# Kernel optimization log

Hardware: AMD Instinct MI355X
Metric: run time of the kernel (lower is better)

## Reference

```python
import jax, jax.numpy as jnp
import numpy as np

M, N, P, T = 8000, 63, 64, 5


def setup_inputs() -> dict:
    key = jax.random.key(0)
    ks = jax.random.split(key, 19)
    sn = (1.0 / N) ** 0.5
    sp = (1.0 / P) ** 0.5
    f32 = jnp.float32
    return {
        "A": jax.random.normal(ks[0], (1, M, N), f32),
        "b": jax.random.normal(ks[1], (1, M), f32),
        "c": jax.random.normal(ks[2], (1, N), f32),
        "theta1r": sn * jax.random.normal(ks[3], (P, N + 1), f32),
        "theta1c": sn * jax.random.normal(ks[4], (P, N + 1), f32),
        "theta2rr": sp * jax.random.normal(ks[5], (P, P), f32),
        "theta2rc": sp * jax.random.normal(ks[6], (P, P), f32),
        "theta2cr": sp * jax.random.normal(ks[7], (P, P), f32),
        "theta3rr": sp * jax.random.normal(ks[8], (P, P), f32),
        "theta3rc": sp * jax.random.normal(ks[9], (P, P), f32),
        "theta3cr": sp * jax.random.normal(ks[10], (P, P), f32),
        "theta4rr": sp * jax.random.normal(ks[11], (P,), f32),
        "theta4rc": sp * jax.random.normal(ks[12], (P,), f32),
        "theta4cr": sp * jax.random.normal(ks[13], (P,), f32),
        "theta6r": sp * jax.random.normal(ks[14], (P, P), f32),
        "theta6c": sp * jax.random.normal(ks[15], (P, P), f32),
        "theta7": sp * jax.random.normal(ks[16], (P, P), f32),
        "W8": 0.05 * jax.random.normal(ks[17], (2, 2 * P), f32),
        "b8": 0.05 * jax.random.normal(ks[18], (2,), f32),
        "z": 7,
    }


def reference(A, b, c, theta1r, theta1c, theta2rr, theta2rc, theta2cr,
              theta3rr, theta3rc, theta3cr, theta4rr, theta4rc, theta4cr,
              theta6r, theta6c, theta7, W8, b8, z):
    relu = jax.nn.relu
    m, n = A.shape[1], A.shape[2]
    p = theta1r.shape[0]
    # raw node features: row node v -> [A[v,:], b[v]]; column node m -> [c, 0]
    Fr_raw = jnp.concatenate([A[0], b[0][:, None]], axis=1)        # (m, n+1)
    fc_raw = jnp.concatenate([c[0], jnp.zeros((1,), A.dtype)])     # (n+1,)
    Fr = Fr_raw / jnp.linalg.norm(Fr_raw, axis=1, keepdims=True)   # f(v), v < m
    fc = fc_raw / jnp.linalg.norm(fc_raw)                          # f(m)
    # edge weights w(v,u) = f(v).f(u) are detached in the original (float(...data))
    Frd = jax.lax.stop_gradient(Fr)
    fcd = jax.lax.stop_gradient(fc)
    Wrr = Frd @ Frd.T                                              # (m, m)
    dg = jnp.diagonal(Wrr)
    srr_pos = relu(Wrr).sum(axis=1) - relu(dg)                     # sum over u != v
    srr_neg = relu(-Wrr).sum(axis=1) - relu(-dg)
    wrc = Frd @ fcd                                                # (m,) = w(v, m)
    # identity: sum_u relu(t4 * w_u) = relu(t4) * sum_u relu(w_u) + relu(-t4) * sum_u relu(-w_u)
    Srr = relu(theta4rr)[:, None] * srr_pos[None, :] + relu(-theta4rr)[:, None] * srr_neg[None, :]
    Src = relu(theta4rc)[:, None] * relu(wrc)[None, :] + relu(-theta4rc)[:, None] * relu(-wrc)[None, :]
    scr = relu(theta4cr) * relu(wrc).sum() + relu(-theta4cr) * relu(-wrc).sum()
    edge_r = theta3rr @ Srr + theta3rc @ Src                       # (p, m), constant over t
    edge_c = theta3cr @ scr                                        # (p,)
    fz = Fr[z]                                                     # z < m: row node feature
    t1r = theta1r @ fz                                             # (p,)
    t1c = theta1c @ fz
    # mu init (p, m+1) = [[Ab^T, c0^T]; 0]; split into row columns / column node
    mu_r0 = jnp.zeros((p, m), A.dtype).at[: n + 1].set(Fr_raw.T)
    mu_c0 = jnp.zeros((p,), A.dtype).at[: n + 1].set(fc_raw)

    def step(carry, _):
        mu_r, mu_c = carry
        # row nodes: term2rr uses old mu[:, v]; term2rc uses old mu[:, m]
        new_r = relu(t1r[:, None] + theta2rr @ mu_r + (theta2rc @ mu_c)[:, None] + edge_r)
        # column node updated last within a sweep -> sees updated row embeddings
        new_c = relu(t1c + theta2cr @ new_r.sum(axis=1) + edge_c)
        return (new_r, new_c), None

    (mu_r, mu_c), _ = jax.lax.scan(step, (mu_r0, mu_c0), None, length=T)
    term6 = theta6r @ mu_r.sum(axis=1) + theta6c @ mu_c            # (p,)
    term7 = theta7 @ mu_r[:, z]                                    # (p,)
    feat = jax.nn.sigmoid(jnp.concatenate([term6, term7]))         # (2p,)
    return (feat @ W8.T + b8)[None, :]                             # (1, 2)
```

## Files before the change

kernel.cpp:

```cpp
#include <hip/hip_runtime.h>
#include <math.h>

typedef __attribute__((ext_vector_type(8))) short short8;
typedef __attribute__((ext_vector_type(4))) float f32x4;

#define WS_SPART 0
#define WS_GPART 262144
#define WS_WPART 294912
#define WS_CPART 295936
#define WS_T1R   335936
#define WS_T1C   336000
#define WS_AL    336064
#define WS_BE    336128
#define WS_GA    336192
#define WS_DE    336256
#define WS_ECP   336320
#define WS_ECN   336384
#define WS_W     336448
#define WS_MUZ   336512
#define WS_WSUM  336576
#define WS_RNORM 336640
#define WS_R2H   344832
#define WS_R2L   346880
#define WS_E4    348928
#define WS_FH    380928
#define WS_FL    643072

__device__ __forceinline__ float waveReduceSum(float v) {
#pragma unroll
    for (int m = 32; m >= 1; m >>= 1) v += __shfl_xor(v, m, 64);
    return v;
}
__device__ __forceinline__ unsigned short f2bf(float f) {
    unsigned int u = __float_as_uint(f);
    unsigned int r = (u + 0x7fffu + ((u >> 16) & 1u)) >> 16;
    return (unsigned short)r;
}
__device__ __forceinline__ float bf2f(unsigned short h) {
    return __uint_as_float(((unsigned int)h) << 16);
}

__global__ __launch_bounds__(256) void k_fr(
    const float* __restrict__ A, const float* __restrict__ b, const float* __restrict__ c,
    const float* __restrict__ th1r, const float* __restrict__ th1c,
    const float* __restrict__ th2rr, const float* __restrict__ th2rc,
    const float* __restrict__ th3rr, const float* __restrict__ th3rc, const float* __restrict__ th3cr,
    const float* __restrict__ th4rr, const float* __restrict__ th4rc, const float* __restrict__ th4cr,
    const int* __restrict__ zp,
    unsigned short* __restrict__ Fh, unsigned short* __restrict__ Fl,
    unsigned short* __restrict__ R2H, unsigned short* __restrict__ R2L,
    float* __restrict__ ws)
{
    int tid = threadIdx.x, lane = tid & 63, wid = tid >> 6;

    if (blockIdx.x == 512) {
        __shared__ float fcraw[64], fz[64], sh4a[64], sh4b[64];
        int p = lane;
        int z = zp[0];
        float cv = (p < 63) ? c[p] : 0.f;
        fcraw[p] = cv;
        float av = (p < 63) ? A[z * 63 + p] : b[z];
        float s2 = waveReduceSum(av * av);
        fz[p] = av * rsqrtf(s2);
        __syncthreads();

        float t1 = 0.f, t2 = 0.f, w0 = 0.f;
#pragma unroll 8
        for (int k = 0; k < 64; k++) {
            t1 += th1r[p * 64 + k] * fz[k];
            t2 += th1c[p * 64 + k] * fz[k];
            w0 += th2rc[p * 64 + k] * fcraw[k];
        }
        ws[WS_T1R + p] = t1;
        ws[WS_T1C + p] = t2;
        ws[WS_W + p] = t1 + w0;

        sh4a[p] = th4rr[p];
        sh4b[p] = th4rc[p];
        __syncthreads();
        float a = 0.f, bb = 0.f, g = 0.f, d = 0.f;
#pragma unroll 8
        for (int k = 0; k < 64; k++) {
            float t4 = sh4a[k];
            a  += th3rr[p * 64 + k] * fmaxf(t4, 0.f);
            bb += th3rr[p * 64 + k] * fmaxf(-t4, 0.f);
            float t5 = sh4b[k];
            g  += th3rc[p * 64 + k] * fmaxf(t5, 0.f);
            d  += th3rc[p * 64 + k] * fmaxf(-t5, 0.f);
        }
        ws[WS_AL + p] = a; ws[WS_BE + p] = bb;
        ws[WS_GA + p] = g; ws[WS_DE + p] = d;
        __syncthreads();
        sh4a[p] = th4cr[p];
        __syncthreads();
        float e1 = 0.f, e2 = 0.f;
#pragma unroll 8
        for (int k = 0; k < 64; k++) {
            float t6 = sh4a[k];
            e1 += th3cr[p * 64 + k] * fmaxf(t6, 0.f);
            e2 += th3cr[p * 64 + k] * fmaxf(-t6, 0.f);
        }
        ws[WS_ECP + p] = e1; ws[WS_ECN + p] = e2;

#pragma unroll
        for (int i = 0; i < 16; i++) {
            int idx = tid * 16 + i;
            float f = th2rr[idx];
            unsigned short h = f2bf(f);
            R2H[idx] = h;
            R2L[idx] = f2bf(f - bf2f(h));
        }
        return;
    }

    __shared__ float gsh[64];
    __shared__ float wsh2[2];
    if (tid < 64) gsh[tid] = 0.f;
    if (tid < 2) wsh2[tid] = 0.f;
    __syncthreads();

    float cv = (lane < 63) ? c[lane] : 0.f;
    float cn2 = waveReduceSum(cv * cv);
    float fcnl = cv * rsqrtf(cn2);

    int r0 = blockIdx.x * 16 + wid * 4;
    float gl = 0.f, lp = 0.f, ln = 0.f;
#pragma unroll
    for (int i = 0; i < 4; i++) {
        int r = r0 + i;
        if (r < 8000) {
            float val = (lane < 63) ? A[r * 63 + lane] : b[r];
            float s2 = waveReduceSum(val * val);
            float f = val * rsqrtf(s2);
            unsigned short h = f2bf(f);
            Fh[r * 64 + lane] = h;
            Fl[r * 64 + lane] = f2bf(f - bf2f(h));
            gl += f;
            float w = waveReduceSum(f * fcnl);
            if (lane == 0) {
                ws[WS_RNORM + r] = sqrtf(s2);
                lp += fmaxf(w, 0.f); ln += fmaxf(-w, 0.f);
            }
        } else {
            Fh[r * 64 + lane] = 0;
            Fl[r * 64 + lane] = 0;
        }
    }
    atomicAdd(&gsh[lane], gl);
    if (lane == 0) { atomicAdd(&wsh2[0], lp); atomicAdd(&wsh2[1], ln); }
    __syncthreads();
    if (tid < 64) ws[WS_GPART + blockIdx.x * 64 + tid] = gsh[tid];
    if (tid == 64) ws[WS_WPART + blockIdx.x * 2 + 0] = wsh2[0];
    if (tid == 65) ws[WS_WPART + blockIdx.x * 2 + 1] = wsh2[1];
}

__global__ __launch_bounds__(256) void k_gram(
    const unsigned short* __restrict__ Fh, float* __restrict__ ws)
{
    int tid = threadIdx.x, lane = tid & 63, wid = tid >> 6;
    int m = lane & 15, quad = lane >> 4;
    int vbase = blockIdx.x * 256 + wid * 64;

    short8 AH[8];
#pragma unroll
    for (int pt = 0; pt < 4; pt++)
#pragma unroll
        for (int q = 0; q < 2; q++)
            AH[pt * 2 + q] = *(const short8*)(Fh + (vbase + pt * 16 + m) * 64 + q * 32 + quad * 8);

    float srr[16];
#pragma unroll
    for (int i = 0; i < 16; i++) srr[i] = 0.f;

    const int y = blockIdx.y;
    const int boff = m * 64 + quad * 8;
    short8 B0[2], B1[2];
#pragma unroll
    for (int q = 0; q < 2; q++)
        B0[q] = *(const short8*)(Fh + y * 16 * 64 + boff + q * 32);

#pragma unroll 1
    for (int k2 = 0; k2 < 8; k2++) {
        int jB1 = y + 32 * (2 * k2 + 1);
#pragma unroll
        for (int q = 0; q < 2; q++)
            B1[q] = *(const short8*)(Fh + jB1 * 16 * 64 + boff + q * 32);
#pragma unroll
        for (int pt = 0; pt < 4; pt++) {
            f32x4 a = {0.f, 0.f, 0.f, 0.f};
            a = __builtin_amdgcn_mfma_f32_16x16x32_bf16(AH[pt * 2 + 0], B0[0], a, 0, 0, 0);
            a = __builtin_amdgcn_mfma_f32_16x16x32_bf16(AH[pt * 2 + 1], B0[1], a, 0, 0, 0);
#pragma unroll
            for (int r = 0; r < 4; r++) srr[pt * 4 + r] += fmaxf(a[r], 0.f);
        }
        if (k2 < 7) {
            int jB0 = y + 32 * (2 * k2 + 2);
#pragma unroll
            for (int q = 0; q < 2; q++)
                B0[q] = *(const short8*)(Fh + jB0 * 16 * 64 + boff + q * 32);
        }
#pragma unroll
        for (int pt = 0; pt < 4; pt++) {
            f32x4 a = {0.f, 0.f, 0.f, 0.f};
            a = __builtin_amdgcn_mfma_f32_16x16x32_bf16(AH[pt * 2 + 0], B1[0], a, 0, 0, 0);
            a = __builtin_amdgcn_mfma_f32_16x16x32_bf16(AH[pt * 2 + 1], B1[1], a, 0, 0, 0);
#pragma unroll
            for (int r = 0; r < 4; r++) srr[pt * 4 + r] += fmaxf(a[r], 0.f);
        }
    }
#pragma unroll
    for (int pt = 0; pt < 4; pt++)
#pragma unroll
        for (int r = 0; r < 4; r++) {
            float s = srr[pt * 4 + r];
            s += __shfl_xor(s, 1, 64); s += __shfl_xor(s, 2, 64);
            s += __shfl_xor(s, 4, 64); s += __shfl_xor(s, 8, 64);
            if (m == 0)
                ws[WS_SPART + y * 8192 + vbase + pt * 16 + quad * 4 + r] = s;
        }
}

__global__ __launch_bounds__(256) void k_mu0(
    const float* __restrict__ c, float* __restrict__ ws,
    unsigned short* __restrict__ MH, unsigned short* __restrict__ ML,
    const unsigned short* __restrict__ R2H, const unsigned short* __restrict__ R2L)
{
    __shared__ float XF[64][68];
    __shared__ float red[256], colp[256];
    __shared__ __align__(16) float wS[64], alS[64], beS[64], gaS[64], deS[64];
    __shared__ float fcnS[64], gS[64], sprow[64];
    __shared__ __align__(16) float e4sh[256];
    int tid = threadIdx.x, lane = tid & 63, wid = tid >> 6;
    int m = lane & 15, quad = lane >> 4;
    int v0 = blockIdx.x * 64;
    int cw = wid * 16 + m;
    int v = v0 + cw;

    if (wid == 0) {
        float cv = (lane < 63) ? c[lane] : 0.f;
        float cn2 = waveReduceSum(cv * cv);
        fcnS[lane] = cv * rsqrtf(cn2);
        wS[lane] = ws[WS_W + lane];
    } else if (wid == 1) {
        alS[lane] = ws[WS_AL + lane]; beS[lane] = ws[WS_BE + lane];
        float wp = 0.f;
#pragma unroll
        for (int k = 0; k < 8; k++) wp += ws[WS_WPART + (lane + 64 * k) * 2];
        wp = waveReduceSum(wp);
        if (lane == 0) ws[WS_WSUM] = wp;
    } else if (wid == 2) {
        gaS[lane] = ws[WS_GA + lane]; deS[lane] = ws[WS_DE + lane];
        float wn = 0.f;
#pragma unroll
        for (int k = 0; k < 8; k++) wn += ws[WS_WPART + (lane + 64 * k) * 2 + 1];
        wn = waveReduceSum(wn);
        if (lane == 0) ws[WS_WSUM + 1] = wn;
    }
    float gv = 0.f;
#pragma unroll 8
    for (int bb = 0; bb < 128; bb++) gv += ws[WS_GPART + (wid * 128 + bb) * 64 + lane];
    red[tid] = gv;
    __syncthreads();
    if (tid < 64) gS[tid] = red[tid] + red[64 + tid] + red[128 + tid] + red[192 + tid];
    __syncthreads();
    float sv = 0.f;
#pragma unroll
    for (int y = wid * 8; y < wid * 8 + 8; y++) sv += ws[WS_SPART + y * 8192 + v0 + lane];
    red[tid] = sv;
    __syncthreads();
    if (tid < 64) sprow[tid] = red[tid] + red[64 + tid] + red[128 + tid] + red[192 + tid];
    __syncthreads();

    for (int i2 = 0; i2 < 16; i2++) {
        int i = wid * 16 + i2;
        int vr = v0 + i;
        float fr = bf2f(MH[vr * 64 + lane]) + bf2f(ML[vr * 64 + lane]);
        float dw = waveReduceSum(fr * fcnS[lane]);
        float dg = waveReduceSum(fr * gS[lane]);
        if (lane == 0) {
            float spv = sprow[i];
            float4 e;
            e.x = spv - 1.0f;
            e.y = spv - dg;
            e.z = fmaxf(dw, 0.f);
            e.w = fmaxf(-dw, 0.f);
            *(float4*)(&e4sh[i * 4]) = e;
            *(float4*)(ws + WS_E4 + vr * 4) = e;
        }
        XF[i][lane] = fr * ws[WS_RNORM + vr];
    }

    short8 RH[8], RL[8];
#pragma unroll
    for (int pt = 0; pt < 4; pt++)
#pragma unroll
        for (int q = 0; q < 2; q++) {
            int off = (pt * 16 + m) * 64 + q * 32 + quad * 8;
            RH[pt * 2 + q] = *(const short8*)(R2H + off);
            RL[pt * 2 + q] = *(const short8*)(R2L + off);
        }
    __syncthreads();

    short8 BH[2], BL[2];
#pragma unroll
    for (int q = 0; q < 2; q++) {
        float4 f0 = *(const float4*)(&XF[cw][q * 32 + quad * 8]);
        float4 f1 = *(const float4*)(&XF[cw][q * 32 + quad * 8 + 4]);
        float xv[8] = {f0.x, f0.y, f0.z, f0.w, f1.x, f1.y, f1.z, f1.w};
        short8 H, L;
#pragma unroll
        for (int j = 0; j < 8; j++) {
            unsigned short h = f2bf(xv[j]);
            H[j] = (short)h;
            L[j] = (short)f2bf(xv[j] - bf2f(h));
        }
        BH[q] = H; BL[q] = L;
    }
    float4 e = *(const float4*)(&e4sh[cw * 4]);

#pragma unroll
    for (int pt = 0; pt < 4; pt++) {
        f32x4 a = {0.f, 0.f, 0.f, 0.f};
#pragma unroll
        for (int q = 0; q < 2; q++) {
            a = __builtin_amdgcn_mfma_f32_16x16x32_bf16(RH[pt*2+q], BH[q], a, 0, 0, 0);
            a = __builtin_amdgcn_mfma_f32_16x16x32_bf16(RH[pt*2+q], BL[q], a, 0, 0, 0);
            a = __builtin_amdgcn_mfma_f32_16x16x32_bf16(RL[pt*2+q], BH[q], a, 0, 0, 0);
        }
        int pbase = pt * 16 + quad * 4;
        float4 w4 = *(const float4*)(wS + pbase);
        float4 a4 = *(const float4*)(alS + pbase);
        float4 b4 = *(const float4*)(beS + pbase);
        float4 g4 = *(const float4*)(gaS + pbase);
        float4 d4 = *(const float4*)(deS + pbase);
        float u0 = fmaxf(a[0] + w4.x + a4.x*e.x + b4.x*e.y + g4.x*e.z + d4.x*e.w, 0.f);
        float u1 = fmaxf(a[1] + w4.y + a4.y*e.x + b4.y*e.y + g4.y*e.z + d4.y*e.w, 0.f);
        float u2 = fmaxf(a[2] + w4.z + a4.z*e.x + b4.z*e.y + g4.z*e.z + d4.z*e.w, 0.f);
        float u3 = fmaxf(a[3] + w4.w + a4.w*e.x + b4.w*e.y + g4.w*e.z + d4.w*e.w, 0.f);
        ushort4 h4, l4;
        h4.x = f2bf(u0); l4.x = f2bf(u0 - bf2f(h4.x));
        h4.y = f2bf(u1); l4.y = f2bf(u1 - bf2f(h4.y));
        h4.z = f2bf(u2); l4.z = f2bf(u2 - bf2f(h4.z));
        h4.w = f2bf(u3); l4.w = f2bf(u3 - bf2f(h4.w));
        *(ushort4*)(MH + v * 64 + pbase) = h4;
        *(ushort4*)(ML + v * 64 + pbase) = l4;
        float c0 = u0, c1 = u1, c2 = u2, c3 = u3;
#pragma unroll
        for (int mm = 1; mm < 16; mm <<= 1) {
            c0 += __shfl_xor(c0, mm, 64);
            c1 += __shfl_xor(c1, mm, 64);
            c2 += __shfl_xor(c2, mm, 64);
            c3 += __shfl_xor(c3, mm, 64);
        }
        if (m == 0) {
            colp[wid * 64 + pbase + 0] = c0;
            colp[wid * 64 + pbase + 1] = c1;
            colp[wid * 64 + pbase + 2] = c2;
            colp[wid * 64 + pbase + 3] = c3;
        }
    }
    __syncthreads();
    if (tid < 64)
        ws[WS_CPART + blockIdx.x * 64 + tid] =
            colp[tid] + colp[64 + tid] + colp[128 + tid] + colp[192 + tid];
}

__global__ __launch_bounds__(256) void k_mu(
    const float* __restrict__ th2cr, const float* __restrict__ th2rc,
    const int* __restrict__ zp, float* __restrict__ ws,
    unsigned short* __restrict__ MH, unsigned short* __restrict__ ML,
    const unsigned short* __restrict__ R2H, const unsigned short* __restrict__ R2L,
    int t)
{
    __shared__ float red[256], colp[256];
    __shared__ __align__(16) float wS[64], alS[64], beS[64], gaS[64], deS[64];
    __shared__ float Ssh[64], ysh[64];
    int tid = threadIdx.x, lane = tid & 63, wid = tid >> 6;
    int m = lane & 15, quad = lane >> 4;
    int v = (blockIdx.x * 4 + wid) * 16 + m;
    int z = zp[0];

    if (tid < 64) {
        alS[tid] = ws[WS_AL + tid]; beS[tid] = ws[WS_BE + tid];
        gaS[tid] = ws[WS_GA + tid]; deS[tid] = ws[WS_DE + tid];
    }
    float s = 0.f;
    for (int blk = wid; blk < 125; blk += 4)
        s += ws[WS_CPART + (t - 1) * 8000 + blk * 64 + lane];
    red[tid] = s;
    __syncthreads();
    if (tid < 64) Ssh[tid] = red[tid] + red[64 + tid] + red[128 + tid] + red[192 + tid];
    __syncthreads();
    {
        int p = wid * 16 + m;
        float acc = 0.f;
        const float4* rowp = (const float4*)(th2cr + p * 64 + quad * 16);
#pragma unroll
        for (int kk = 0; kk < 4; kk++) {
            float4 r4 = rowp[kk];
            acc += r4.x * Ssh[quad * 16 + 4 * kk]     + r4.y * Ssh[quad * 16 + 4 * kk + 1]
                 + r4.z * Ssh[quad * 16 + 4 * kk + 2] + r4.w * Ssh[quad * 16 + 4 * kk + 3];
        }
        acc += __shfl_xor(acc, 16, 64);
        acc += __shfl_xor(acc, 32, 64);
        if (quad == 0)
            ysh[p] = fmaxf(acc + ws[WS_T1C + p] + ws[WS_WSUM] * ws[WS_ECP + p]
                           + ws[WS_WSUM + 1] * ws[WS_ECN + p], 0.f);
    }
    __syncthreads();
    {
        int p = wid * 16 + m;
        float acc = 0.f;
        const float4* rowp = (const float4*)(th2rc + p * 64 + quad * 16);
#pragma unroll
        for (int kk = 0; kk < 4; kk++) {
            float4 r4 = rowp[kk];
            acc += r4.x * ysh[quad * 16 + 4 * kk]     + r4.y * ysh[quad * 16 + 4 * kk + 1]
                 + r4.z * ysh[quad * 16 + 4 * kk + 2] + r4.w * ysh[quad * 16 + 4 * kk + 3];
        }
        acc += __shfl_xor(acc, 16, 64);
        acc += __shfl_xor(acc, 32, 64);
        if (quad == 0) wS[p] = acc + ws[WS_T1R + p];
    }

    short8 RH[8], RL[8];
#pragma unroll
    for (int pt = 0; pt < 4; pt++)
#pragma unroll
        for (int q = 0; q < 2; q++) {
            int off = (pt * 16 + m) * 64 + q * 32 + quad * 8;
            RH[pt * 2 + q] = *(const short8*)(R2H + off);
            RL[pt * 2 + q] = *(const short8*)(R2L + off);
        }
    short8 BH[2], BL[2];
#pragma unroll
    for (int q = 0; q < 2; q++) {
        BH[q] = *(const short8*)(MH + v * 64 + q * 32 + quad * 8);
        BL[q] = *(const short8*)(ML + v * 64 + q * 32 + quad * 8);
    }
    float4 e = *(const float4*)(ws + WS_E4 + v * 4);
    __syncthreads();

#pragma unroll
    for (int pt = 0; pt < 4; pt++) {
        f32x4 a = {0.f, 0.f, 0.f, 0.f};
#pragma unroll
        for (int q = 0; q < 2; q++) {
            a = __builtin_amdgcn_mfma_f32_16x16x32_bf16(RH[pt*2+q], BH[q], a, 0, 0, 0);
            a = __builtin_amdgcn_mfma_f32_16x16x32_bf16(RH[pt*2+q], BL[q], a, 0, 0, 0);
            a = __builtin_amdgcn_mfma_f32_16x16x32_bf16(RL[pt*2+q], BH[q], a, 0, 0, 0);
        }
        int pbase = pt * 16 + quad * 4;
        float4 w4 = *(const float4*)(wS + pbase);
        float4 a4 = *(const float4*)(alS + pbase);
        float4 b4 = *(const float4*)(beS + pbase);
        float4 g4 = *(const float4*)(gaS + pbase);
        float4 d4 = *(const float4*)(deS + pbase);
        float u0 = fmaxf(a[0] + w4.x + a4.x*e.x + b4.x*e.y + g4.x*e.z + d4.x*e.w, 0.f);
        float u1 = fmaxf(a[1] + w4.y + a4.y*e.x + b4.y*e.y + g4.y*e.z + d4.y*e.w, 0.f);
        float u2 = fmaxf(a[2] + w4.z + a4.z*e.x + b4.z*e.y + g4.z*e.z + d4.z*e.w, 0.f);
        float u3 = fmaxf(a[3] + w4.w + a4.w*e.x + b4.w*e.y + g4.w*e.z + d4.w*e.w, 0.f);
        ushort4 h4, l4;
        h4.x = f2bf(u0); l4.x = f2bf(u0 - bf2f(h4.x));
        h4.y = f2bf(u1); l4.y = f2bf(u1 - bf2f(h4.y));
        h4.z = f2bf(u2); l4.z = f2bf(u2 - bf2f(h4.z));
        h4.w = f2bf(u3); l4.w = f2bf(u3 - bf2f(h4.w));
        *(ushort4*)(MH + v * 64 + pbase) = h4;
        *(ushort4*)(ML + v * 64 + pbase) = l4;
        float c0 = u0, c1 = u1, c2 = u2, c3 = u3;
#pragma unroll
        for (int mm = 1; mm < 16; mm <<= 1) {
            c0 += __shfl_xor(c0, mm, 64);
            c1 += __shfl_xor(c1, mm, 64);
            c2 += __shfl_xor(c2, mm, 64);
            c3 += __shfl_xor(c3, mm, 64);
        }
        if (m == 0) {
            colp[wid * 64 + pbase + 0] = c0;
            colp[wid * 64 + pbase + 1] = c1;
            colp[wid * 64 + pbase + 2] = c2;
            colp[wid * 64 + pbase + 3] = c3;
        }
        if (t == 4 && v == z) {
            float4 o; o.x = u0; o.y = u1; o.z = u2; o.w = u3;
            *(float4*)(ws + WS_MUZ + pbase) = o;
        }
    }
    __syncthreads();
    if (tid < 64)
        ws[WS_CPART + t * 8000 + blockIdx.x * 64 + tid] =
            colp[tid] + colp[64 + tid] + colp[128 + tid] + colp[192 + tid];
}

__global__ __launch_bounds__(256) void k_head(
    const float* __restrict__ th2cr,
    const float* __restrict__ th6r, const float* __restrict__ th6c,
    const float* __restrict__ th7, const float* __restrict__ W8,
    const float* __restrict__ b8,
    float* __restrict__ ws, float* __restrict__ out)
{
    __shared__ float red[256], Ssh[64], ysh[64], feat[128];
    int tid = threadIdx.x, lane = tid & 63, wid = tid >> 6;

    float s = 0.f;
    for (int blk = wid; blk < 125; blk += 4)
        s += ws[WS_CPART + 4 * 8000 + blk * 64 + lane];
    red[tid] = s;
    __syncthreads();
    if (tid < 64) Ssh[tid] = red[tid] + red[64 + tid] + red[128 + tid] + red[192 + tid];
    __syncthreads();
    int p = tid;
    if (p < 64) {
        float acc = ws[WS_T1C + p] + ws[WS_WSUM] * ws[WS_ECP + p]
                  + ws[WS_WSUM + 1] * ws[WS_ECN + p];
#pragma unroll 8
        for (int k = 0; k < 64; k++) acc += th2cr[p * 64 + k] * Ssh[k];
        ysh[p] = fmaxf(acc, 0.f);
    }
    __syncthreads();
    if (p < 64) {
        float t6 = 0.f, t7 = 0.f;
#pragma unroll 8
        for (int k = 0; k < 64; k++) {
            t6 += th6r[p * 64 + k] * Ssh[k] + th6c[p * 64 + k] * ysh[k];
            t7 += th7[p * 64 + k] * ws[WS_MUZ + k];
        }
        feat[p] = 1.f / (1.f + expf(-t6));
        feat[64 + p] = 1.f / (1.f + expf(-t7));
    }
    __syncthreads();
    if (p < 2) {
        float o = b8[p];
        for (int i = 0; i < 128; i++) o += W8[p * 128 + i] * feat[i];
        out[p] = o;
    }
}

extern "C" void kernel_launch(void* const* d_in, const int* in_sizes, int n_in,
                              void* d_out, int out_size, void* d_ws, size_t ws_size,
                              hipStream_t stream) {
    (void)in_sizes; (void)n_in; (void)out_size; (void)ws_size;
    const float* A     = (const float*)d_in[0];
    const float* b     = (const float*)d_in[1];
    const float* c     = (const float*)d_in[2];
    const float* th1r  = (const float*)d_in[3];
    const float* th1c  = (const float*)d_in[4];
    const float* th2rr = (const float*)d_in[5];
    const float* th2rc = (const float*)d_in[6];
    const float* th2cr = (const float*)d_in[7];
    const float* th3rr = (const float*)d_in[8];
    const float* th3rc = (const float*)d_in[9];
    const float* th3cr = (const float*)d_in[10];
    const float* th4rr = (const float*)d_in[11];
    const float* th4rc = (const float*)d_in[12];
    const float* th4cr = (const float*)d_in[13];
    const float* th6r  = (const float*)d_in[14];
    const float* th6c  = (const float*)d_in[15];
    const float* th7   = (const float*)d_in[16];
    const float* W8    = (const float*)d_in[17];
    const float* b8    = (const float*)d_in[18];
    const int*   zp    = (const int*)d_in[19];
    float* ws  = (float*)d_ws;
    float* out = (float*)d_out;
    unsigned short* Fh  = (unsigned short*)(ws + WS_FH);
    unsigned short* Fl  = (unsigned short*)(ws + WS_FL);
    unsigned short* R2H = (unsigned short*)(ws + WS_R2H);
    unsigned short* R2L = (unsigned short*)(ws + WS_R2L);

    k_fr<<<513, 256, 0, stream>>>(A, b, c, th1r, th1c, th2rr, th2rc, th3rr, th3rc,
                                  th3cr, th4rr, th4rc, th4cr, zp, Fh, Fl, R2H, R2L, ws);
    k_gram<<<dim3(32, 32), 256, 0, stream>>>(Fh, ws);
    k_mu0<<<125, 256, 0, stream>>>(c, ws, Fh, Fl, R2H, R2L);
    for (int t = 1; t < 5; t++)
        k_mu<<<125, 256, 0, stream>>>(th2cr, th2rc, zp, ws, Fh, Fl, R2H, R2L, t);
    k_head<<<1, 256, 0, stream>>>(th2cr, th6r, th6c, th7, W8, b8, ws, out);
}
```

Before: 226.0 us.

## Fuse mu iterations and head into one cooperative kernel with grid sync

```diff
diff --git a/kernel.cpp b/kernel.cpp
--- a/kernel.cpp
+++ b/kernel.cpp
@@ -1,4 +1,5 @@
 #include <hip/hip_runtime.h>
+#include <hip/hip_cooperative_groups.h>
 #include <math.h>
 
 typedef __attribute__((ext_vector_type(8))) short short8;
@@ -220,21 +221,42 @@
         }
 }
 
-__global__ __launch_bounds__(256) void k_mu0(
-    const float* __restrict__ c, float* __restrict__ ws,
+__global__ __launch_bounds__(256) void k_mu_fused(
+    const float* __restrict__ c,
+    const float* __restrict__ th2cr, const float* __restrict__ th2rc,
+    const float* __restrict__ th6r, const float* __restrict__ th6c,
+    const float* __restrict__ th7, const float* __restrict__ W8,
+    const float* __restrict__ b8, const int* __restrict__ zp,
+    float* __restrict__ ws,
     unsigned short* __restrict__ MH, unsigned short* __restrict__ ML,
-    const unsigned short* __restrict__ R2H, const unsigned short* __restrict__ R2L)
+    const unsigned short* __restrict__ R2H, const unsigned short* __restrict__ R2L,
+    float* __restrict__ out)
 {
+    cooperative_groups::grid_group grid = cooperative_groups::this_grid();
+
     __shared__ float XF[64][68];
     __shared__ float red[256], colp[256];
     __shared__ __align__(16) float wS[64], alS[64], beS[64], gaS[64], deS[64];
     __shared__ float fcnS[64], gS[64], sprow[64];
     __shared__ __align__(16) float e4sh[256];
+    __shared__ float Ssh[64], ysh[64], feat[128];
+
     int tid = threadIdx.x, lane = tid & 63, wid = tid >> 6;
     int m = lane & 15, quad = lane >> 4;
     int v0 = blockIdx.x * 64;
     int cw = wid * 16 + m;
     int v = v0 + cw;
+    int z = zp[0];
+
+    short8 RH[8], RL[8];
+#pragma unroll
+    for (int pt = 0; pt < 4; pt++)
+#pragma unroll
+        for (int q = 0; q < 2; q++) {
+            int off = (pt * 16 + m) * 64 + q * 32 + quad * 8;
+            RH[pt * 2 + q] = *(const short8*)(R2H + off);
+            RL[pt * 2 + q] = *(const short8*)(R2L + off);
+        }
 
     if (wid == 0) {
         float cv = (lane < 63) ? c[lane] : 0.f;
@@ -279,26 +301,15 @@
         float dg = waveReduceSum(fr * gS[lane]);
         if (lane == 0) {
             float spv = sprow[i];
-            float4 e;
-            e.x = spv - 1.0f;
-            e.y = spv - dg;
-            e.z = fmaxf(dw, 0.f);
-            e.w = fmaxf(-dw, 0.f);
-            *(float4*)(&e4sh[i * 4]) = e;
-            *(float4*)(ws + WS_E4 + vr * 4) = e;
+            float4 ee;
+            ee.x = spv - 1.0f;
+            ee.y = spv - dg;
+            ee.z = fmaxf(dw, 0.f);
+            ee.w = fmaxf(-dw, 0.f);
+            *(float4*)(&e4sh[i * 4]) = ee;
         }
         XF[i][lane] = fr * ws[WS_RNORM + vr];
     }
-
-    short8 RH[8], RL[8];
-#pragma unroll
-    for (int pt = 0; pt < 4; pt++)
-#pragma unroll
-        for (int q = 0; q < 2; q++) {
-            int off = (pt * 16 + m) * 64 + q * 32 + quad * 8;
-            RH[pt * 2 + q] = *(const short8*)(R2H + off);
-            RL[pt * 2 + q] = *(const short8*)(R2L + off);
-        }
     __syncthreads();
 
     short8 BH[2], BL[2];
@@ -318,189 +329,119 @@
     }
     float4 e = *(const float4*)(&e4sh[cw * 4]);
 
-#pragma unroll
-    for (int pt = 0; pt < 4; pt++) {
-        f32x4 a = {0.f, 0.f, 0.f, 0.f};
+    auto mu_core = [&](const short8* BHl, const short8* BLl, int t) {
+#pragma unroll
+        for (int pt = 0; pt < 4; pt++) {
+            f32x4 a = {0.f, 0.f, 0.f, 0.f};
+#pragma unroll
+            for (int q = 0; q < 2; q++) {
+                a = __builtin_amdgcn_mfma_f32_16x16x32_bf16(RH[pt*2+q], BHl[q], a, 0, 0, 0);
+                a = __builtin_amdgcn_mfma_f32_16x16x32_bf16(RH[pt*2+q], BLl[q], a, 0, 0, 0);
+                a = __builtin_amdgcn_mfma_f32_16x16x32_bf16(RL[pt*2+q], BHl[q], a, 0, 0, 0);
+            }
+            int pbase = pt * 16 + quad * 4;
+            float4 w4 = *(const float4*)(wS + pbase);
+            float4 a4 = *(const float4*)(alS + pbase);
+            float4 b4 = *(const float4*)(beS + pbase);
+            float4 g4 = *(const float4*)(gaS + pbase);
+            float4 d4 = *(const float4*)(deS + pbase);
+            float u0 = fmaxf(a[0] + w4.x + a4.x*e.x + b4.x*e.y + g4.x*e.z + d4.x*e.w, 0.f);
+            float u1 = fmaxf(a[1] + w4.y + a4.y*e.x + b4.y*e.y + g4.y*e.z + d4.y*e.w, 0.f);
+            float u2 = fmaxf(a[2] + w4.z + a4.z*e.x + b4.z*e.y + g4.z*e.z + d4.z*e.w, 0.f);
+            float u3 = fmaxf(a[3] + w4.w + a4.w*e.x + b4.w*e.y + g4.w*e.z + d4.w*e.w, 0.f);
+            if (t < 4) {
+                ushort4 h4, l4;
+                h4.x = f2bf(u0); l4.x = f2bf(u0 - bf2f(h4.x));
+                h4.y = f2bf(u1); l4.y = f2bf(u1 - bf2f(h4.y));
+                h4.z = f2bf(u2); l4.z = f2bf(u2 - bf2f(h4.z));
+                h4.w = f2bf(u3); l4.w = f2bf(u3 - bf2f(h4.w));
+                *(ushort4*)(MH + v * 64 + pbase) = h4;
+                *(ushort4*)(ML + v * 64 + pbase) = l4;
+            }
+            if (t == 4 && v == z) {
+                float4 o; o.x = u0; o.y = u1; o.z = u2; o.w = u3;
+                *(float4*)(ws + WS_MUZ + pbase) = o;
+            }
+            float c0 = u0, c1 = u1, c2 = u2, c3 = u3;
+#pragma unroll
+            for (int mm = 1; mm < 16; mm <<= 1) {
+                c0 += __shfl_xor(c0, mm, 64);
+                c1 += __shfl_xor(c1, mm, 64);
+                c2 += __shfl_xor(c2, mm, 64);
+                c3 += __shfl_xor(c3, mm, 64);
+            }
+            if (m == 0) {
+                colp[wid * 64 + pbase + 0] = c0;
+                colp[wid * 64 + pbase + 1] = c1;
+                colp[wid * 64 + pbase + 2] = c2;
+                colp[wid * 64 + pbase + 3] = c3;
+            }
+        }
+        __syncthreads();
+        if (tid < 64)
+            ws[WS_CPART + t * 8000 + blockIdx.x * 64 + tid] =
+                colp[tid] + colp[64 + tid] + colp[128 + tid] + colp[192 + tid];
+    };
+
+    mu_core(BH, BL, 0);
+
+    for (int t = 1; t <= 4; t++) {
+        __threadfence();
+        grid.sync();
+        __threadfence();
+
+        float s = 0.f;
+        for (int blk = wid; blk < 125; blk += 4)
+            s += ws[WS_CPART + (t - 1) * 8000 + blk * 64 + lane];
+        red[tid] = s;
+        __syncthreads();
+        if (tid < 64) Ssh[tid] = red[tid] + red[64 + tid] + red[128 + tid] + red[192 + tid];
+        __syncthreads();
+        {
+            int p = wid * 16 + m;
+            float acc = 0.f;
+            const float4* rowp = (const float4*)(th2cr + p * 64 + quad * 16);
+#pragma unroll
+            for (int kk = 0; kk < 4; kk++) {
+                float4 r4 = rowp[kk];
+                acc += r4.x * Ssh[quad * 16 + 4 * kk]     + r4.y * Ssh[quad * 16 + 4 * kk + 1]
+                     + r4.z * Ssh[quad * 16 + 4 * kk + 2] + r4.w * Ssh[quad * 16 + 4 * kk + 3];
+            }
+            acc += __shfl_xor(acc, 16, 64);
+            acc += __shfl_xor(acc, 32, 64);
+            if (quad == 0)
+                ysh[p] = fmaxf(acc + ws[WS_T1C + p] + ws[WS_WSUM] * ws[WS_ECP + p]
+                               + ws[WS_WSUM + 1] * ws[WS_ECN + p], 0.f);
+        }
+        __syncthreads();
+        {
+            int p = wid * 16 + m;
+            float acc = 0.f;
+            const float4* rowp = (const float4*)(th2rc + p * 64 + quad * 16);
+#pragma unroll
+            for (int kk = 0; kk < 4; kk++) {
+                float4 r4 = rowp[kk];
+                acc += r4.x * ysh[quad * 16 + 4 * kk]     + r4.y * ysh[quad * 16 + 4 * kk + 1]
+                     + r4.z * ysh[quad * 16 + 4 * kk + 2] + r4.w * ysh[quad * 16 + 4 * kk + 3];
+            }
+            acc += __shfl_xor(acc, 16, 64);
+            acc += __shfl_xor(acc, 32, 64);
+            if (quad == 0) wS[p] = acc + ws[WS_T1R + p];
+        }
+        short8 BHs[2], BLs[2];
 #pragma unroll
         for (int q = 0; q < 2; q++) {
-            a = __builtin_amdgcn_mfma_f32_16x16x32_bf16(RH[pt*2+q], BH[q], a, 0, 0, 0);
-            a = __builtin_amdgcn_mfma_f32_16x16x32_bf16(RH[pt*2+q], BL[q], a, 0, 0, 0);
-            a = __builtin_amdgcn_mfma_f32_16x16x32_bf16(RL[pt*2+q], BH[q], a, 0, 0, 0);
-        }
-        int pbase = pt * 16 + quad * 4;
-        float4 w4 = *(const float4*)(wS + pbase);
-        float4 a4 = *(const float4*)(alS + pbase);
-        float4 b4 = *(const float4*)(beS + pbase);
-        float4 g4 = *(const float4*)(gaS + pbase);
-        float4 d4 = *(const float4*)(deS + pbase);
-        float u0 = fmaxf(a[0] + w4.x + a4.x*e.x + b4.x*e.y + g4.x*e.z + d4.x*e.w, 0.f);
-        float u1 = fmaxf(a[1] + w4.y + a4.y*e.x + b4.y*e.y + g4.y*e.z + d4.y*e.w, 0.f);
-        float u2 = fmaxf(a[2] + w4.z + a4.z*e.x + b4.z*e.y + g4.z*e.z + d4.z*e.w, 0.f);
-        float u3 = fmaxf(a[3] + w4.w + a4.w*e.x + b4.w*e.y + g4.w*e.z + d4.w*e.w, 0.f);
-        ushort4 h4, l4;
-        h4.x = f2bf(u0); l4.x = f2bf(u0 - bf2f(h4.x));
-        h4.y = f2bf(u1); l4.y = f2bf(u1 - bf2f(h4.y));
-        h4.z = f2bf(u2); l4.z = f2bf(u2 - bf2f(h4.z));
-        h4.w = f2bf(u3); l4.w = f2bf(u3 - bf2f(h4.w));
-        *(ushort4*)(MH + v * 64 + pbase) = h4;
-        *(ushort4*)(ML + v * 64 + pbase) = l4;
-        float c0 = u0, c1 = u1, c2 = u2, c3 = u3;
-#pragma unroll
-        for (int mm = 1; mm < 16; mm <<= 1) {
-            c0 += __shfl_xor(c0, mm, 64);
-            c1 += __shfl_xor(c1, mm, 64);
-            c2 += __shfl_xor(c2, mm, 64);
-            c3 += __shfl_xor(c3, mm, 64);
-        }
-        if (m == 0) {
-            colp[wid * 64 + pbase + 0] = c0;
-            colp[wid * 64 + pbase + 1] = c1;
-            colp[wid * 64 + pbase + 2] = c2;
-            colp[wid * 64 + pbase + 3] = c3;
-        }
-    }
-    __syncthreads();
-    if (tid < 64)
-        ws[WS_CPART + blockIdx.x * 64 + tid] =
-            colp[tid] + colp[64 + tid] + colp[128 + tid] + colp[192 + tid];
-}
-
-__global__ __launch_bounds__(256) void k_mu(
-    const float* __restrict__ th2cr, const float* __restrict__ th2rc,
-    const int* __restrict__ zp, float* __restrict__ ws,
-    unsigned short* __restrict__ MH, unsigned short* __restrict__ ML,
-    const unsigned short* __restrict__ R2H, const unsigned short* __restrict__ R2L,
-    int t)
-{
-    __shared__ float red[256], colp[256];
-    __shared__ __align__(16) float wS[64], alS[64], beS[64], gaS[64], deS[64];
-    __shared__ float Ssh[64], ysh[64];
-    int tid = threadIdx.x, lane = tid & 63, wid = tid >> 6;
-    int m = lane & 15, quad = lane >> 4;
-    int v = (blockIdx.x * 4 + wid) * 16 + m;
-    int z = zp[0];
-
-    if (tid < 64) {
-        alS[tid] = ws[WS_AL + tid]; beS[tid] = ws[WS_BE + tid];
-        gaS[tid] = ws[WS_GA + tid]; deS[tid] = ws[WS_DE + tid];
-    }
-    float s = 0.f;
-    for (int blk = wid; blk < 125; blk += 4)
-        s += ws[WS_CPART + (t - 1) * 8000 + blk * 64 + lane];
-    red[tid] = s;
-    __syncthreads();
-    if (tid < 64) Ssh[tid] = red[tid] + red[64 + tid] + red[128 + tid] + red[192 + tid];
-    __syncthreads();
-    {
-        int p = wid * 16 + m;
-        float acc = 0.f;
-        const float4* rowp = (const float4*)(th2cr + p * 64 + quad * 16);
-#pragma unroll
-        for (int kk = 0; kk < 4; kk++) {
-            float4 r4 = rowp[kk];
-            acc += r4.x * Ssh[quad * 16 + 4 * kk]     + r4.y * Ssh[quad * 16 + 4 * kk + 1]
-                 + r4.z * Ssh[quad * 16 + 4 * kk + 2] + r4.w * Ssh[quad * 16 + 4 * kk + 3];
-        }
-        acc += __shfl_xor(acc, 16, 64);
-        acc += __shfl_xor(acc, 32, 64);
-        if (quad == 0)
-            ysh[p] = fmaxf(acc + ws[WS_T1C + p] + ws[WS_WSUM] * ws[WS_ECP + p]
-                           + ws[WS_WSUM + 1] * ws[WS_ECN + p], 0.f);
-    }
-    __syncthreads();
-    {
-        int p = wid * 16 + m;
-        float acc = 0.f;
-        const float4* rowp = (const float4*)(th2rc + p * 64 + quad * 16);
-#pragma unroll
-        for (int kk = 0; kk < 4; kk++) {
-            float4 r4 = rowp[kk];
-            acc += r4.x * ysh[quad * 16 + 4 * kk]     + r4.y * ysh[quad * 16 + 4 * kk + 1]
-                 + r4.z * ysh[quad * 16 + 4 * kk + 2] + r4.w * ysh[quad * 16 + 4 * kk + 3];
-        }
-        acc += __shfl_xor(acc, 16, 64);
-        acc += __shfl_xor(acc, 32, 64);
-        if (quad == 0) wS[p] = acc + ws[WS_T1R + p];
-    }
-
-    short8 RH[8], RL[8];
-#pragma unroll
-    for (int pt = 0; pt < 4; pt++)
-#pragma unroll
-        for (int q = 0; q < 2; q++) {
-            int off = (pt * 16 + m) * 64 + q * 32 + quad * 8;
-            RH[pt * 2 + q] = *(const short8*)(R2H + off);
-            RL[pt * 2 + q] = *(const short8*)(R2L + off);
-        }
-    short8 BH[2], BL[2];
-#pragma unroll
-    for (int q = 0; q < 2; q++) {
-        BH[q] = *(const short8*)(MH + v * 64 + q * 32 + quad * 8);
-        BL[q] = *(const short8*)(ML + v * 64 + q * 32 + quad * 8);
-    }
-    float4 e = *(const float4*)(ws + WS_E4 + v * 4);
-    __syncthreads();
-
-#pragma unroll
-    for (int pt = 0; pt < 4; pt++) {
-        f32x4 a = {0.f, 0.f, 0.f, 0.f};
-#pragma unroll
-        for (int q = 0; q < 2; q++) {
-            a = __builtin_amdgcn_mfma_f32_16x16x32_bf16(RH[pt*2+q], BH[q], a, 0, 0, 0);
-            a = __builtin_amdgcn_mfma_f32_16x16x32_bf16(RH[pt*2+q], BL[q], a, 0, 0, 0);
-            a = __builtin_amdgcn_mfma_f32_16x16x32_bf16(RL[pt*2+q], BH[q], a, 0, 0, 0);
-        }
-        int pbase = pt * 16 + quad * 4;
-        float4 w4 = *(const float4*)(wS + pbase);
-        float4 a4 = *(const float4*)(alS + pbase);
-        float4 b4 = *(const float4*)(beS + pbase);
-        float4 g4 = *(const float4*)(gaS + pbase);
-        float4 d4 = *(const float4*)(deS + pbase);
-        float u0 = fmaxf(a[0] + w4.x + a4.x*e.x + b4.x*e.y + g4.x*e.z + d4.x*e.w, 0.f);
-        float u1 = fmaxf(a[1] + w4.y + a4.y*e.x + b4.y*e.y + g4.y*e.z + d4.y*e.w, 0.f);
-        float u2 = fmaxf(a[2] + w4.z + a4.z*e.x + b4.z*e.y + g4.z*e.z + d4.z*e.w, 0.f);
-        float u3 = fmaxf(a[3] + w4.w + a4.w*e.x + b4.w*e.y + g4.w*e.z + d4.w*e.w, 0.f);
-        ushort4 h4, l4;
-        h4.x = f2bf(u0); l4.x = f2bf(u0 - bf2f(h4.x));
-        h4.y = f2bf(u1); l4.y = f2bf(u1 - bf2f(h4.y));
-        h4.z = f2bf(u2); l4.z = f2bf(u2 - bf2f(h4.z));
-        h4.w = f2bf(u3); l4.w = f2bf(u3 - bf2f(h4.w));
-        *(ushort4*)(MH + v * 64 + pbase) = h4;
-        *(ushort4*)(ML + v * 64 + pbase) = l4;
-        float c0 = u0, c1 = u1, c2 = u2, c3 = u3;
-#pragma unroll
-        for (int mm = 1; mm < 16; mm <<= 1) {
-            c0 += __shfl_xor(c0, mm, 64);
-            c1 += __shfl_xor(c1, mm, 64);
-            c2 += __shfl_xor(c2, mm, 64);
-            c3 += __shfl_xor(c3, mm, 64);
-        }
-        if (m == 0) {
-            colp[wid * 64 + pbase + 0] = c0;
-            colp[wid * 64 + pbase + 1] = c1;
-            colp[wid * 64 + pbase + 2] = c2;
-            colp[wid * 64 + pbase + 3] = c3;
-        }
-        if (t == 4 && v == z) {
-            float4 o; o.x = u0; o.y = u1; o.z = u2; o.w = u3;
-            *(float4*)(ws + WS_MUZ + pbase) = o;
-        }
-    }
-    __syncthreads();
-    if (tid < 64)
-        ws[WS_CPART + t * 8000 + blockIdx.x * 64 + tid] =
-            colp[tid] + colp[64 + tid] + colp[128 + tid] + colp[192 + tid];
-}
-
-__global__ __launch_bounds__(256) void k_head(
-    const float* __restrict__ th2cr,
-    const float* __restrict__ th6r, const float* __restrict__ th6c,
-    const float* __restrict__ th7, const float* __restrict__ W8,
-    const float* __restrict__ b8,
-    float* __restrict__ ws, float* __restrict__ out)
-{
-    __shared__ float red[256], Ssh[64], ysh[64], feat[128];
-    int tid = threadIdx.x, lane = tid & 63, wid = tid >> 6;
+            BHs[q] = *(const short8*)(MH + v * 64 + q * 32 + quad * 8);
+            BLs[q] = *(const short8*)(ML + v * 64 + q * 32 + quad * 8);
+        }
+        __syncthreads();
+        mu_core(BHs, BLs, t);
+    }
+
+    __threadfence();
+    grid.sync();
+    if (blockIdx.x != 0) return;
+    __threadfence();
 
     float s = 0.f;
     for (int blk = wid; blk < 125; blk += 4)
@@ -570,8 +511,12 @@
     k_fr<<<513, 256, 0, stream>>>(A, b, c, th1r, th1c, th2rr, th2rc, th3rr, th3rc,
                                   th3cr, th4rr, th4rc, th4cr, zp, Fh, Fl, R2H, R2L, ws);
     k_gram<<<dim3(32, 32), 256, 0, stream>>>(Fh, ws);
-    k_mu0<<<125, 256, 0, stream>>>(c, ws, Fh, Fl, R2H, R2L);
-    for (int t = 1; t < 5; t++)
-        k_mu<<<125, 256, 0, stream>>>(th2cr, th2rc, zp, ws, Fh, Fl, R2H, R2L, t);
-    k_head<<<1, 256, 0, stream>>>(th2cr, th6r, th6c, th7, W8, b8, ws, out);
-}
+    {
+        void* kargs[] = {
+            (void*)&c, (void*)&th2cr, (void*)&th2rc, (void*)&th6r, (void*)&th6c,
+            (void*)&th7, (void*)&W8, (void*)&b8, (void*)&zp, (void*)&ws,
+            (void*)&Fh, (void*)&Fl, (void*)&R2H, (void*)&R2L, (void*)&out };
+        hipLaunchCooperativeKernel((const void*)k_mu_fused, dim3(125), dim3(256),
+                                   kargs, 0, stream);
+    }
+}
```

After: 408.2 us. 1.81x slower.
